# Kernel tuning notes

Measured on AMD Instinct MI355X. Metric: run time of the kernel, lower is better.

The kernel has to match this reference:

```python
import jax, jax.numpy as jnp
import numpy as np

D = 1024  # dim_context


def setup_inputs() -> dict:
    key = jax.random.key(0)
    k1, k2, k3, k4, k5 = jax.random.split(key, 5)
    B, T = 32, 2048
    hidden = jax.random.normal(k1, (B, D), dtype=jnp.float32)
    encoder_outputs = jax.random.normal(k2, (B, T, D), dtype=jnp.float32)
    # nn.Linear(2D, D): weight [D, 2D], bias [D]
    lim = 1.0 / np.sqrt(2 * D)
    W = jax.random.uniform(k3, (D, 2 * D), minval=-lim, maxval=lim, dtype=jnp.float32)
    b = jax.random.uniform(k4, (D,), minval=-lim, maxval=lim, dtype=jnp.float32)
    stdv = 1.0 / np.sqrt(D)
    v = jax.random.uniform(k5, (D,), minval=-stdv, maxval=stdv, dtype=jnp.float32)
    return {"hidden": hidden, "encoder_outputs": encoder_outputs, "W": W, "b": b, "v": v}


def reference(hidden, encoder_outputs, W, b, v):
    # hidden: [B, D]; encoder_outputs: [B, T, D]
    B, T, Dm = encoder_outputs.shape
    h = jnp.broadcast_to(hidden[:, None, :], (B, T, Dm))      # repeat over T
    attn_inputs = jnp.concatenate([h, encoder_outputs], axis=2)  # [B, T, 2D]
    energy = jax.nn.relu(jnp.einsum('btk,dk->btd', attn_inputs, W) + b)  # [B, T, D]
    scores = jnp.einsum('btd,d->bt', energy, v)                # [B, T]
    # softmax over dim=1 (time axis), then unsqueeze(1)
    return jax.nn.softmax(scores, axis=1)[:, None, :]          # [B, 1, T]
```

## Files before the change

### kernel.cpp

```cpp
#include <hip/hip_runtime.h>
#include <cstdint>


#define GLOBAL_AS __attribute__((address_space(1)))
#define LDS_AS    __attribute__((address_space(3)))

typedef __bf16 bf16x8 __attribute__((ext_vector_type(8)));
typedef float  f32x4  __attribute__((ext_vector_type(4)));

__device__ __forceinline__ unsigned int f2bf(float x) {
    unsigned int u = __builtin_bit_cast(unsigned int, x);
    u += 0x7fffu + ((u >> 16) & 1u);
    return u >> 16;
}

__global__ __launch_bounds__(256) void k_convert_enc(const float4* __restrict__ in,
                                                     uint4* __restrict__ out) {
    size_t idx = (size_t)blockIdx.x * 256 + threadIdx.x;
    float4 f0 = in[idx * 2];
    float4 f1 = in[idx * 2 + 1];
    uint4 o;
    o.x = f2bf(f0.x) | (f2bf(f0.y) << 16);
    o.y = f2bf(f0.z) | (f2bf(f0.w) << 16);
    o.z = f2bf(f1.x) | (f2bf(f1.y) << 16);
    o.w = f2bf(f1.z) | (f2bf(f1.w) << 16);
    out[idx] = o;
}

__global__ __launch_bounds__(256) void k_convert_we(const float* __restrict__ W,
                                                    uint2* __restrict__ out) {
    int idx = blockIdx.x * 256 + threadIdx.x;
    int i = idx * 4;
    int n = i >> 10, k = i & 1023;
    const float4 f = *(const float4*)(W + (size_t)n * 2048 + 1024 + k);
    uint2 o;
    o.x = f2bf(f.x) | (f2bf(f.y) << 16);
    o.y = f2bf(f.z) | (f2bf(f.w) << 16);
    out[idx] = o;
}

__global__ __launch_bounds__(256) void k_hidden_proj(const float* __restrict__ hidden,
                                                     const float* __restrict__ W,
                                                     const float* __restrict__ bias,
                                                     float* __restrict__ u) {
    __shared__ float wrow[1024];
    __shared__ float red[256];
    const int tid = threadIdx.x, d = blockIdx.x;
    ((float4*)wrow)[tid] = ((const float4*)(W + (size_t)d * 2048))[tid];
    __syncthreads();
    const int b = tid & 31, kc = tid >> 5;
    const float* h = hidden + b * 1024 + kc * 128;
    const float* w = wrow + kc * 128;
    float acc = 0.f;
    #pragma unroll 8
    for (int i = 0; i < 128; i += 4) {
        float4 hv = *(const float4*)(h + i);
        acc += w[i] * hv.x + w[i + 1] * hv.y + w[i + 2] * hv.z + w[i + 3] * hv.w;
    }
    red[tid] = acc;
    __syncthreads();
    if (tid < 32) {
        float s = 0.f;
        #pragma unroll
        for (int j = 0; j < 8; j++) s += red[j * 32 + tid];
        u[tid * 1024 + d] = s + bias[d];
    }
}


#define STAGE_A(S, h, kk) do {                                                          \
    __builtin_amdgcn_global_load_lds(                                                   \
        (GLOBAL_AS void*)(size_t)(Ab + arow0 + (kk) + (h) * 32),                        \
        (LDS_AS void*)(&As[S][h][c0 * 512]), 16, 0, 0);                                 \
    __builtin_amdgcn_global_load_lds(                                                   \
        (GLOBAL_AS void*)(size_t)(Ab + arow1 + (kk) + (h) * 32),                        \
        (LDS_AS void*)(&As[S][h][c0 * 512 + 512]), 16, 0, 0);                           \
} while (0)

#define STAGE_B(S, h, kk) do {                                                          \
    __builtin_amdgcn_global_load_lds(                                                   \
        (GLOBAL_AS void*)(size_t)(Bbase + brow0 + (kk) + (h) * 32),                     \
        (LDS_AS void*)(&Bs[S][h][c0 * 512]), 16, 0, 0);                                 \
    __builtin_amdgcn_global_load_lds(                                                   \
        (GLOBAL_AS void*)(size_t)(Bbase + brow1 + (kk) + (h) * 32),                     \
        (LDS_AS void*)(&Bs[S][h][c0 * 512 + 512]), 16, 0, 0);                           \
} while (0)

#define PHASE_MFMA(jp)                                                                  \
    __builtin_amdgcn_s_barrier();                                                       \
    asm volatile("s_waitcnt lgkmcnt(0)" ::: "memory");                                  \
    __builtin_amdgcn_sched_barrier(0);                                                  \
    __builtin_amdgcn_s_setprio(1);                                                      \
    _Pragma("unroll")                                                                   \
    for (int i = 0; i < 8; i++) {                                                       \
        acc[i][2 * (jp)]     = __builtin_amdgcn_mfma_f32_16x16x32_bf16(                 \
            afr[i], bfr[0], acc[i][2 * (jp)], 0, 0, 0);                                 \
        acc[i][2 * (jp) + 1] = __builtin_amdgcn_mfma_f32_16x16x32_bf16(                 \
            afr[i], bfr[1], acc[i][2 * (jp) + 1], 0, 0, 0);                             \
    }                                                                                   \
    __builtin_amdgcn_s_setprio(0);                                                      \
    __builtin_amdgcn_s_barrier();

#define TILE(C, S, kst) do {                                                            \
    {                                                               \
        const unsigned short* Ap = As[C][0];                                            \
        const unsigned short* Bp = Bs[C][0];                                            \
        _Pragma("unroll")                                                               \
        for (int i = 0; i < 8; i++) afr[i] = *(const bf16x8*)(Ap + aBase + i * 512);    \
        bfr[0] = *(const bf16x8*)(Bp + bBase);                                          \
        bfr[1] = *(const bf16x8*)(Bp + bBase + 512);                                    \
        STAGE_A(S, 0, kst);                                                             \
        PHASE_MFMA(0)                                                                   \
    }                                                                                   \
    {                                                               \
        const unsigned short* Bp = Bs[C][0];                                            \
        bfr[0] = *(const bf16x8*)(Bp + bBase + 1024);                                   \
        bfr[1] = *(const bf16x8*)(Bp + bBase + 1536);                                   \
        STAGE_B(S, 0, kst);                                                             \
        asm volatile("s_waitcnt vmcnt(4)" ::: "memory");                                \
        PHASE_MFMA(1)                                                                   \
    }                                                                                   \
    {                                                               \
        const unsigned short* Ap = As[C][1];                                            \
        const unsigned short* Bp = Bs[C][1];                                            \
        _Pragma("unroll")                                                               \
        for (int i = 0; i < 8; i++) afr[i] = *(const bf16x8*)(Ap + aBase + i * 512);    \
        bfr[0] = *(const bf16x8*)(Bp + bBase);                                          \
        bfr[1] = *(const bf16x8*)(Bp + bBase + 512);                                    \
        STAGE_A(S, 1, kst);                                                             \
        PHASE_MFMA(0)                                                                   \
    }                                                                                   \
    {                                                               \
        const unsigned short* Bp = Bs[C][1];                                            \
        bfr[0] = *(const bf16x8*)(Bp + bBase + 1024);                                   \
        bfr[1] = *(const bf16x8*)(Bp + bBase + 1536);                                   \
        STAGE_B(S, 1, kst);                                                             \
        asm volatile("s_waitcnt vmcnt(4)" ::: "memory");                                \
        PHASE_MFMA(1)                                                                   \
    }                                                                                   \
} while (0)

__global__ __launch_bounds__(512, 2) void k_gemm_score(
        const unsigned short* __restrict__ Ab,
        const unsigned short* __restrict__ Bw,
        const float* __restrict__ u,
        const float* __restrict__ v,
        float* __restrict__ scores4) {
    __shared__ __align__(16) unsigned short As[2][2][8192];
    __shared__ __align__(16) unsigned short Bs[2][2][8192];
    __shared__ float red[4][256];

    const int tid  = threadIdx.x;
    const int wave = tid >> 6;
    const int lane = tid & 63;
    const int bid  = blockIdx.x;
    const int lg   = (bid & 7) * 128 + (bid >> 3);
    const int mb   = lg >> 2;
    const int nb   = lg & 3;
    const int wm = wave & 1, wn = wave >> 1;
    const int q = lane >> 4, cl = lane & 15;
    const int bidx = mb >> 3;

    const int perm  = (q ^ ((cl >> 1) & 3)) << 3;
    const int aBase = (wm * 128 + cl) * 32 + perm;
    const int bBase = (wn * 64 + cl) * 32 + perm;

    const int c0 = wave * 2;
    const int g8 = (((lane & 3) ^ ((lane >> 3) & 3)) << 3);
    const int rowA0 = c0 * 16 + (lane >> 2);
    const size_t arow0 = (size_t)(mb * 256 + rowA0) * 1024 + g8;
    const size_t arow1 = arow0 + 16 * 1024;
    const size_t brow0 = (size_t)rowA0 * 1024 + g8;
    const size_t brow1 = brow0 + 16 * 1024;
    const unsigned short* Bbase = Bw + (size_t)nb * 262144;

    f32x4 acc[8][4];
    bf16x8 afr[8], bfr[2];
    #pragma unroll
    for (int i = 0; i < 8; i++)
        #pragma unroll
        for (int j = 0; j < 4; j++) acc[i][j] = (f32x4){0.f, 0.f, 0.f, 0.f};

    STAGE_A(0, 0, 0);
    STAGE_B(0, 0, 0);
    STAGE_A(0, 1, 0);
    STAGE_B(0, 1, 0);
    asm volatile("s_waitcnt vmcnt(4)" ::: "memory");
    __builtin_amdgcn_s_barrier();

    for (int it = 0; it < 8; it++) {
        const int k1 = (2 * it + 1) * 64;
        TILE(0, 1, k1);
        const int k2 = (it == 7) ? 0 : (2 * it + 2) * 64;
        TILE(1, 0, k2);
    }

    float vv[4], uu[4];
    #pragma unroll
    for (int j = 0; j < 4; j++) {
        int n = nb * 256 + wn * 64 + j * 16 + cl;
        vv[j] = v[n];
        uu[j] = u[bidx * 1024 + n];
    }
    #pragma unroll
    for (int i = 0; i < 8; i++)
        #pragma unroll
        for (int r = 0; r < 4; r++) {
            float s = 0.f;
            #pragma unroll
            for (int j = 0; j < 4; j++)
                s += fmaxf(acc[i][j][r] + uu[j], 0.f) * vv[j];
            s += __shfl_xor(s, 1);
            s += __shfl_xor(s, 2);
            s += __shfl_xor(s, 4);
            s += __shfl_xor(s, 8);
            if (cl == 0) red[wn][wm * 128 + i * 16 + q * 4 + r] = s;
        }
    __syncthreads();
    if (tid < 256) {
        scores4[(size_t)nb * 65536 + mb * 256 + tid] =
            red[0][tid] + red[1][tid] + red[2][tid] + red[3][tid];
    }
}

__global__ __launch_bounds__(256) void k_softmax(const float* __restrict__ scores4,
                                                 float* __restrict__ out) {
    __shared__ float red[4];
    int b = blockIdx.x;
    int t0 = threadIdx.x;
    int wave = threadIdx.x >> 6, lane = threadIdx.x & 63;
    const float* s0 = scores4 + b * 2048;
    float vals[8];
    float lmax = -1e30f;
    #pragma unroll
    for (int i = 0; i < 8; i++) {
        int t = t0 + i * 256;
        vals[i] = s0[t] + s0[65536 + t] + s0[131072 + t] + s0[196608 + t];
        lmax = fmaxf(lmax, vals[i]);
    }
    for (int o = 32; o > 0; o >>= 1) lmax = fmaxf(lmax, __shfl_xor(lmax, o));
    if (lane == 0) red[wave] = lmax;
    __syncthreads();
    float gmax = fmaxf(fmaxf(red[0], red[1]), fmaxf(red[2], red[3]));
    float lsum = 0.f;
    #pragma unroll
    for (int i = 0; i < 8; i++) {
        vals[i] = expf(vals[i] - gmax);
        lsum += vals[i];
    }
    for (int o = 32; o > 0; o >>= 1) lsum += __shfl_xor(lsum, o);
    __syncthreads();
    if (lane == 0) red[wave] = lsum;
    __syncthreads();
    float inv = 1.0f / (red[0] + red[1] + red[2] + red[3]);
    #pragma unroll
    for (int i = 0; i < 8; i++) out[b * 2048 + t0 + i * 256] = vals[i] * inv;
}

extern "C" void kernel_launch(void* const* d_in, const int* in_sizes, int n_in,
                              void* d_out, int out_size, void* d_ws, size_t ws_size,
                              hipStream_t stream) {
    const float* hidden = (const float*)d_in[0];
    const float* enc    = (const float*)d_in[1];
    const float* W      = (const float*)d_in[2];
    const float* bias   = (const float*)d_in[3];
    const float* v      = (const float*)d_in[4];
    float* out = (float*)d_out;

    char* ws = (char*)d_ws;
    unsigned short* encb = (unsigned short*)ws;
    unsigned short* Web  = (unsigned short*)(ws + 134217728);
    float* u       = (float*)(ws + 134217728 + 2097152);
    float* scores4 = (float*)(ws + 134217728 + 2097152 + 131072);

    k_convert_enc<<<32768, 256, 0, stream>>>((const float4*)enc, (uint4*)encb);
    k_convert_we<<<1024, 256, 0, stream>>>(W, (uint2*)Web);
    k_hidden_proj<<<1024, 256, 0, stream>>>(hidden, W, bias, u);
    k_gemm_score<<<1024, 512, 0, stream>>>(encb, Web, u, v, scores4);
    k_softmax<<<32, 256, 0, stream>>>(scores4, out);
}
```

Baseline: 570.3 us.

## Fuse encoder fp32-to-bf16 conversion into GEMM A-tile loading via registers

```diff
diff --git a/kernel.cpp b/kernel.cpp
--- a/kernel.cpp
+++ b/kernel.cpp
@@ -12,19 +12,6 @@
     unsigned int u = __builtin_bit_cast(unsigned int, x);
     u += 0x7fffu + ((u >> 16) & 1u);
     return u >> 16;
-}
-
-__global__ __launch_bounds__(256) void k_convert_enc(const float4* __restrict__ in,
-                                                     uint4* __restrict__ out) {
-    size_t idx = (size_t)blockIdx.x * 256 + threadIdx.x;
-    float4 f0 = in[idx * 2];
-    float4 f1 = in[idx * 2 + 1];
-    uint4 o;
-    o.x = f2bf(f0.x) | (f2bf(f0.y) << 16);
-    o.y = f2bf(f0.z) | (f2bf(f0.w) << 16);
-    o.z = f2bf(f1.x) | (f2bf(f1.y) << 16);
-    o.w = f2bf(f1.z) | (f2bf(f1.w) << 16);
-    out[idx] = o;
 }
 
 __global__ __launch_bounds__(256) void k_convert_we(const float* __restrict__ W,
@@ -68,13 +55,25 @@
 }
 
 
-#define STAGE_A(S, h, kk) do {                                                          \
-    __builtin_amdgcn_global_load_lds(                                                   \
-        (GLOBAL_AS void*)(size_t)(Ab + arow0 + (kk) + (h) * 32),                        \
-        (LDS_AS void*)(&As[S][h][c0 * 512]), 16, 0, 0);                                 \
-    __builtin_amdgcn_global_load_lds(                                                   \
-        (GLOBAL_AS void*)(size_t)(Ab + arow1 + (kk) + (h) * 32),                        \
-        (LDS_AS void*)(&As[S][h][c0 * 512 + 512]), 16, 0, 0);                           \
+#define A_LOAD(h, kk) do {                                                              \
+    aL[h][0] = *(const float4*)(Af + arow0 + (kk) + (h) * 32);                          \
+    aL[h][1] = *(const float4*)(Af + arow0 + (kk) + (h) * 32 + 4);                      \
+    aL[h][2] = *(const float4*)(Af + arow1 + (kk) + (h) * 32);                          \
+    aL[h][3] = *(const float4*)(Af + arow1 + (kk) + (h) * 32 + 4);                      \
+} while (0)
+
+#define A_WRITE(S, h) do {                                                              \
+    bf16x8 w0, w1;                                                                      \
+    w0[0] = (__bf16)aL[h][0].x; w0[1] = (__bf16)aL[h][0].y;                             \
+    w0[2] = (__bf16)aL[h][0].z; w0[3] = (__bf16)aL[h][0].w;                             \
+    w0[4] = (__bf16)aL[h][1].x; w0[5] = (__bf16)aL[h][1].y;                             \
+    w0[6] = (__bf16)aL[h][1].z; w0[7] = (__bf16)aL[h][1].w;                             \
+    w1[0] = (__bf16)aL[h][2].x; w1[1] = (__bf16)aL[h][2].y;                             \
+    w1[2] = (__bf16)aL[h][2].z; w1[3] = (__bf16)aL[h][2].w;                             \
+    w1[4] = (__bf16)aL[h][3].x; w1[5] = (__bf16)aL[h][3].y;                             \
+    w1[6] = (__bf16)aL[h][3].z; w1[7] = (__bf16)aL[h][3].w;                             \
+    *(bf16x8*)(&As[S][h][c0 * 512 + lane * 8])       = w0;                              \
+    *(bf16x8*)(&As[S][h][c0 * 512 + 512 + lane * 8]) = w1;                              \
 } while (0)
 
 #define STAGE_B(S, h, kk) do {                                                          \
@@ -102,46 +101,49 @@
     __builtin_amdgcn_s_barrier();
 
 #define TILE(C, S, kst) do {                                                            \
-    {                                                               \
+    {                                    \
         const unsigned short* Ap = As[C][0];                                            \
         const unsigned short* Bp = Bs[C][0];                                            \
         _Pragma("unroll")                                                               \
         for (int i = 0; i < 8; i++) afr[i] = *(const bf16x8*)(Ap + aBase + i * 512);    \
         bfr[0] = *(const bf16x8*)(Bp + bBase);                                          \
         bfr[1] = *(const bf16x8*)(Bp + bBase + 512);                                    \
-        STAGE_A(S, 0, kst);                                                             \
+        A_LOAD(0, kst);                                                                 \
         PHASE_MFMA(0)                                                                   \
     }                                                                                   \
-    {                                                               \
+    {                           \
         const unsigned short* Bp = Bs[C][0];                                            \
         bfr[0] = *(const bf16x8*)(Bp + bBase + 1024);                                   \
         bfr[1] = *(const bf16x8*)(Bp + bBase + 1536);                                   \
         STAGE_B(S, 0, kst);                                                             \
-        asm volatile("s_waitcnt vmcnt(4)" ::: "memory");                                \
+        A_LOAD(1, kst);                                                                 \
+        asm volatile("s_waitcnt vmcnt(10)" ::: "memory");                               \
         PHASE_MFMA(1)                                                                   \
     }                                                                                   \
-    {                                                               \
+    {                                              \
         const unsigned short* Ap = As[C][1];                                            \
         const unsigned short* Bp = Bs[C][1];                                            \
         _Pragma("unroll")                                                               \
         for (int i = 0; i < 8; i++) afr[i] = *(const bf16x8*)(Ap + aBase + i * 512);    \
         bfr[0] = *(const bf16x8*)(Bp + bBase);                                          \
         bfr[1] = *(const bf16x8*)(Bp + bBase + 512);                                    \
-        STAGE_A(S, 1, kst);                                                             \
+        asm volatile("s_waitcnt vmcnt(6)" ::: "memory");                                \
+        A_WRITE(S, 0);                                                                  \
         PHASE_MFMA(0)                                                                   \
     }                                                                                   \
-    {                                                               \
+    {                                  \
         const unsigned short* Bp = Bs[C][1];                                            \
         bfr[0] = *(const bf16x8*)(Bp + bBase + 1024);                                   \
         bfr[1] = *(const bf16x8*)(Bp + bBase + 1536);                                   \
         STAGE_B(S, 1, kst);                                                             \
-        asm volatile("s_waitcnt vmcnt(4)" ::: "memory");                                \
+        asm volatile("s_waitcnt vmcnt(2)" ::: "memory");                                \
+        A_WRITE(S, 1);                                                                  \
         PHASE_MFMA(1)                                                                   \
     }                                                                                   \
 } while (0)
 
 __global__ __launch_bounds__(512, 2) void k_gemm_score(
-        const unsigned short* __restrict__ Ab,
+        const float* __restrict__ Af,
         const unsigned short* __restrict__ Bw,
         const float* __restrict__ u,
         const float* __restrict__ v,
@@ -176,16 +178,20 @@
 
     f32x4 acc[8][4];
     bf16x8 afr[8], bfr[2];
+    float4 aL[2][4];
     #pragma unroll
     for (int i = 0; i < 8; i++)
         #pragma unroll
         for (int j = 0; j < 4; j++) acc[i][j] = (f32x4){0.f, 0.f, 0.f, 0.f};
 
-    STAGE_A(0, 0, 0);
+    A_LOAD(0, 0);
+    A_LOAD(1, 0);
     STAGE_B(0, 0, 0);
-    STAGE_A(0, 1, 0);
     STAGE_B(0, 1, 0);
-    asm volatile("s_waitcnt vmcnt(4)" ::: "memory");
+    asm volatile("s_waitcnt vmcnt(0)" ::: "memory");
+    A_WRITE(0, 0);
+    A_WRITE(0, 1);
+    asm volatile("s_waitcnt lgkmcnt(0)" ::: "memory");
     __builtin_amdgcn_s_barrier();
 
     for (int it = 0; it < 8; it++) {
@@ -268,14 +274,12 @@
     float* out = (float*)d_out;
 
     char* ws = (char*)d_ws;
-    unsigned short* encb = (unsigned short*)ws;
-    unsigned short* Web  = (unsigned short*)(ws + 134217728);
-    float* u       = (float*)(ws + 134217728 + 2097152);
-    float* scores4 = (float*)(ws + 134217728 + 2097152 + 131072);
-
-    k_convert_enc<<<32768, 256, 0, stream>>>((const float4*)enc, (uint4*)encb);
+    unsigned short* Web  = (unsigned short*)ws;
+    float* u       = (float*)(ws + 2097152);
+    float* scores4 = (float*)(ws + 2097152 + 131072);
+
     k_convert_we<<<1024, 256, 0, stream>>>(W, (uint2*)Web);
     k_hidden_proj<<<1024, 256, 0, stream>>>(hidden, W, bias, u);
-    k_gemm_score<<<1024, 512, 0, stream>>>(encb, Web, u, v, scores4);
+    k_gemm_score<<<1024, 512, 0, stream>>>(enc, Web, u, v, scores4);
     k_softmax<<<32, 256, 0, stream>>>(scores4, out);
 }
```

New measurement: 587.1 us. 2.9% more time.
